# Kernel tuning notes

Measured on AMD Instinct MI355X. Metric: run time of the kernel, lower is better.

The kernel has to match this reference:

```python
import jax, jax.numpy as jnp
import numpy as np

FP8_MAX = 448.0


def _quantize_fp8(x):
    """Per-tensor symmetric quantization matching the Triton kernel's decode.

    Encode: u = round(clip(x*scale, -448, 448) / 448 * 127)  (stored as u+128 in uint8)
    Decode: x_hat = u / 127 * 448 / scale,  with scale = 448 / amax(|x|).
    We keep u as a float array of integers in [-127, 127] (the +128 uint8 bias
    cancels in the kernel's `u - 128`).
    """
    amax = jnp.max(jnp.abs(x))
    scale = FP8_MAX / jnp.maximum(amax, jnp.asarray(1e-12, x.dtype))
    q = jnp.clip(x * scale, -FP8_MAX, FP8_MAX)
    u = jnp.round(q / FP8_MAX * 127.0)
    return u, scale


def reference(x, weight):
    orig_shape = x.shape
    K = weight.shape[1]
    x2d = x.reshape(-1, K)                      # [M, K]

    ua, a_scale = _quantize_fp8(x2d)            # codes + per-tensor scale
    uw, w_scale = _quantize_fp8(weight)         # weight: [N, K]

    # Kernel dequant: val = u / 127 * FP8_MAX; acc in fp32; rescale by 1/(a_scale*b_scale)
    a_f = ua * (FP8_MAX / 127.0)
    b_f = (uw * (FP8_MAX / 127.0)).T            # [K, N] (weight_fp8.t())
    acc = a_f @ b_f                              # fp32 accumulate, [M, N]
    out = acc * (1.0 / (a_scale * w_scale))
    out = out.astype(x.dtype)
    return out.reshape(*orig_shape[:-1], weight.shape[0])


def setup_inputs() -> dict:
    key = jax.random.key(0)
    k1, k2 = jax.random.split(key)
    x = jax.random.normal(k1, (4, 2048, 4096), dtype=jnp.float32)
    weight = jax.random.normal(k2, (8192, 4096), dtype=jnp.float32) * 0.02
    return {"x": x, "weight": weight}
```

## Files before the change

kernel.cpp:

```cpp
#include <hip/hip_runtime.h>

#define FP8_MAX_F 448.0f

static constexpr int M = 8192;
static constexpr int N = 8192;
static constexpr int K = 4096;

typedef __attribute__((ext_vector_type(4))) int i32x4;

#define AS1 __attribute__((address_space(1)))
#define AS3 __attribute__((address_space(3)))
#define BARRIER() asm volatile("s_barrier" ::: "memory")
#define VMCNT(n)  asm volatile("s_waitcnt vmcnt(" #n ")" ::: "memory")

__global__ void amax_kernel(const float* __restrict__ x, const float* __restrict__ w,
                            unsigned* __restrict__ out) {
    const long n4x = (long)M * K / 4;
    const long n4t = n4x + (long)N * K / 4;
    unsigned lx = 0u, lw = 0u;
    const long stride = (long)gridDim.x * blockDim.x;
    for (long i = (long)blockIdx.x * blockDim.x + threadIdx.x; i < n4t; i += stride) {
        if (i < n4x) {
            float4 v = ((const float4*)x)[i];
            unsigned a0 = __float_as_uint(v.x) & 0x7fffffffu;
            unsigned a1 = __float_as_uint(v.y) & 0x7fffffffu;
            unsigned a2 = __float_as_uint(v.z) & 0x7fffffffu;
            unsigned a3 = __float_as_uint(v.w) & 0x7fffffffu;
            lx = max(lx, max(max(a0, a1), max(a2, a3)));
        } else {
            float4 v = ((const float4*)w)[i - n4x];
            unsigned a0 = __float_as_uint(v.x) & 0x7fffffffu;
            unsigned a1 = __float_as_uint(v.y) & 0x7fffffffu;
            unsigned a2 = __float_as_uint(v.z) & 0x7fffffffu;
            unsigned a3 = __float_as_uint(v.w) & 0x7fffffffu;
            lw = max(lw, max(max(a0, a1), max(a2, a3)));
        }
    }
    #pragma unroll
    for (int off = 32; off > 0; off >>= 1) {
        lx = max(lx, (unsigned)__shfl_down((int)lx, off, 64));
        lw = max(lw, (unsigned)__shfl_down((int)lw, off, 64));
    }
    __shared__ unsigned smx[4], smw[4];
    if ((threadIdx.x & 63) == 0) { smx[threadIdx.x >> 6] = lx; smw[threadIdx.x >> 6] = lw; }
    __syncthreads();
    if (threadIdx.x == 0) {
        atomicMax(&out[0], max(max(smx[0], smx[1]), max(smx[2], smx[3])));
        atomicMax(&out[1], max(max(smw[0], smw[1]), max(smw[2], smw[3])));
    }
}

__device__ __forceinline__ signed char quant1(float v, float s) {
    float f = fminf(fmaxf(v * s, -FP8_MAX_F), FP8_MAX_F);
    return (signed char)(int)rintf(f / FP8_MAX_F * 127.0f);
}

__global__ void quant_kernel(const float* __restrict__ x, const float* __restrict__ w,
                             signed char* __restrict__ qx, signed char* __restrict__ qw,
                             const unsigned* __restrict__ amax_bits) {
    const float ax = fmaxf(__uint_as_float(amax_bits[0]), 1e-12f);
    const float aw = fmaxf(__uint_as_float(amax_bits[1]), 1e-12f);
    const float sxv = FP8_MAX_F / ax;
    const float swv = FP8_MAX_F / aw;
    const long cx = (long)M * K / 16;
    const long ct = cx + (long)N * K / 16;
    const long stride = (long)gridDim.x * blockDim.x;
    for (long ci = (long)blockIdx.x * blockDim.x + threadIdx.x; ci < ct; ci += stride) {
        const float* src; signed char* dst; float s; long c;
        if (ci < cx) { src = x; dst = qx; s = sxv; c = ci; }
        else         { src = w; dst = qw; s = swv; c = ci - cx; }
        const long r = c >> 8;
        const int  cr = (int)(c & 255);
        const float4* in = (const float4*)(src + r * K + cr * 16);
        signed char ob[16];
        #pragma unroll
        for (int j = 0; j < 4; ++j) {
            float4 v = in[j];
            ob[j * 4 + 0] = quant1(v.x, s);
            ob[j * 4 + 1] = quant1(v.y, s);
            ob[j * 4 + 2] = quant1(v.z, s);
            ob[j * 4 + 3] = quant1(v.w, s);
        }
        const int osub = (cr & 3) ^ ((int)(r >> 1) & 3);
        *(int4*)(dst + r * K + ((long)((cr & ~3) + osub)) * 16) = *(const int4*)ob;
    }
}

__global__ __launch_bounds__(512, 2) void gemm_i8_kernel(
    const signed char* __restrict__ Aq, const signed char* __restrict__ Bq,
    float* __restrict__ C, const unsigned* __restrict__ amax_bits)
{
    __shared__ signed char lds[4][2][256 * 64];

    const int tid  = threadIdx.x;
    const int wid  = tid >> 6;
    const int lane = tid & 63;
    const int wm = wid >> 2;
    const int wn = wid & 3;
    const int fr = lane & 15;
    const int fq = lane >> 4;

    const long row0 = (long)blockIdx.x * 256;
    const long col0 = (long)blockIdx.y * 256;

    const signed char* Ablk = Aq + row0 * K;
    const signed char* Bblk = Bq + col0 * K;

    const long stag_off = (long)(tid >> 2) * K + (long)(tid & 3) * 16;

    const int arow = wm * 128 + fr;
    const int aoff = arow * 64 + ((fq ^ ((arow >> 1) & 3)) * 16);
    const int brow = wn * 64 + fr;
    const int boff = brow * 64 + ((fq ^ ((brow >> 1) & 3)) * 16);

    i32x4 acc[8][4] = {};

#define STAGE(gbase, lbase) do { \
        __builtin_amdgcn_global_load_lds((const AS1 void*)((gbase) + stag_off), \
            (AS3 void*)((lbase) + wid * 1024), 16, 0, 0); \
        __builtin_amdgcn_global_load_lds((const AS1 void*)((gbase) + stag_off + 128L * K), \
            (AS3 void*)((lbase) + 8192 + wid * 1024), 16, 0, 0); \
    } while (0)

#define MFMA8(nb, bA, bB) do { \
        _Pragma("unroll") \
        for (int mi = 0; mi < 8; ++mi) { \
            acc[mi][nb]     = __builtin_amdgcn_mfma_i32_16x16x64_i8(af[mi], bA, acc[mi][nb], 0, 0, 0); \
            acc[mi][nb + 1] = __builtin_amdgcn_mfma_i32_16x16x64_i8(af[mi], bB, acc[mi][nb + 1], 0, 0, 0); \
        } \
    } while (0)

#define TILE(bufi, STAGE_A_STMT, STAGE_B_STMT, VM_B_STMT) do { \
        const signed char* la = &lds[bufi][0][0]; \
        const signed char* lb = &lds[bufi][1][0]; \
        i32x4 af[8], b0, b1, b2, b3; \
        STAGE_A_STMT; \
        _Pragma("unroll") \
        for (int mi = 0; mi < 8; ++mi) \
            af[mi] = *(const i32x4*)(la + aoff + mi * 1024); \
        b0 = *(const i32x4*)(lb + boff + 0 * 1024); \
        b1 = *(const i32x4*)(lb + boff + 1 * 1024); \
        BARRIER(); \
        __builtin_amdgcn_s_setprio(1); \
        MFMA8(0, b0, b1); \
        __builtin_amdgcn_s_setprio(0); \
        BARRIER(); \
        STAGE_B_STMT; \
        b2 = *(const i32x4*)(lb + boff + 2 * 1024); \
        b3 = *(const i32x4*)(lb + boff + 3 * 1024); \
        VM_B_STMT; \
        BARRIER(); \
        __builtin_amdgcn_s_setprio(1); \
        MFMA8(2, b2, b3); \
        __builtin_amdgcn_s_setprio(0); \
        BARRIER(); \
    } while (0)

    STAGE(Ablk + 0 * 64, &lds[0][0][0]);
    STAGE(Bblk + 0 * 64, &lds[0][1][0]);
    STAGE(Ablk + 1 * 64, &lds[1][0][0]);
    STAGE(Bblk + 1 * 64, &lds[1][1][0]);
    VMCNT(4);
    BARRIER();

    #pragma unroll 1
    for (int t = 0; t <= 60; t += 2) {
        TILE(t & 3,
             STAGE(Ablk + (t + 2) * 64, &lds[(t + 2) & 3][0][0]),
             STAGE(Bblk + (t + 2) * 64, &lds[(t + 2) & 3][1][0]),
             VMCNT(4));
        TILE((t + 1) & 3,
             STAGE(Ablk + (t + 3) * 64, &lds[(t + 3) & 3][0][0]),
             STAGE(Bblk + (t + 3) * 64, &lds[(t + 3) & 3][1][0]),
             VMCNT(4));
    }
    TILE(2, (void)0, (void)0, VMCNT(0));
    TILE(3, (void)0, (void)0, (void)0);

#undef TILE
#undef MFMA8
#undef STAGE

    const float ax = fmaxf(__uint_as_float(amax_bits[0]), 1e-12f);
    const float aw = fmaxf(__uint_as_float(amax_bits[1]), 1e-12f);
    const float factor = ax * aw * (1.0f / (127.0f * 127.0f));

    #pragma unroll
    for (int mi = 0; mi < 8; ++mi) {
        #pragma unroll
        for (int ni = 0; ni < 4; ++ni) {
            const long col = col0 + wn * 64 + ni * 16 + fr;
            #pragma unroll
            for (int j = 0; j < 4; ++j) {
                const long row = row0 + wm * 128 + mi * 16 + fq * 4 + j;
                C[row * N + col] = (float)acc[mi][ni][j] * factor;
            }
        }
    }
}

extern "C" void kernel_launch(void* const* d_in, const int* in_sizes, int n_in,
                              void* d_out, int out_size, void* d_ws, size_t ws_size,
                              hipStream_t stream) {
    const float* x = (const float*)d_in[0];
    const float* w = (const float*)d_in[1];
    float* out = (float*)d_out;

    unsigned char* ws = (unsigned char*)d_ws;
    unsigned* amax = (unsigned*)ws;
    signed char* aq = (signed char*)(ws + 256);
    signed char* wq = aq + (long)M * K;

    hipMemsetAsync(amax, 0, 2 * sizeof(unsigned), stream);
    amax_kernel<<<2048, 256, 0, stream>>>(x, w, amax);
    quant_kernel<<<4096, 256, 0, stream>>>(x, w, aq, wq, amax);

    dim3 grid(M / 256, N / 256);
    gemm_i8_kernel<<<grid, 512, 0, stream>>>(aq, wq, out, amax);
}
```

Baseline: 419.1 us.

## Double-buffer LDS fragments in registers and deepen the global prefetch pipeline

The GEMM main loop now keeps two register sets of A/B fragments, loading the next k-tile's fragments from LDS while the MFMAs consume the current set, and prefetches three k-tiles ahead into the 4-slot LDS ring instead of two. This is meant to hide LDS read latency behind the MFMAs and give the global-to-LDS loads more slack. In exchange it roughly doubles fragment register usage, which risks spills under launch_bounds(512,2). The tail now issues redundant wrapped loads (indices masked with &63) instead of separate epilogue tiles, and the waitcnt depth may not match the deeper prefetch.

After: 419.4 us. About the same (+0.1%).

```diff
diff --git a/kernel.cpp b/kernel.cpp
--- a/kernel.cpp
+++ b/kernel.cpp
@@ -102,7 +102,6 @@
 
     const long row0 = (long)blockIdx.x * 256;
     const long col0 = (long)blockIdx.y * 256;
-
     const signed char* Ablk = Aq + row0 * K;
     const signed char* Bblk = Bq + col0 * K;
 
@@ -114,72 +113,78 @@
     const int boff = brow * 64 + ((fq ^ ((brow >> 1) & 3)) * 16);
 
     i32x4 acc[8][4] = {};
-
-#define STAGE(gbase, lbase) do { \
-        __builtin_amdgcn_global_load_lds((const AS1 void*)((gbase) + stag_off), \
-            (AS3 void*)((lbase) + wid * 1024), 16, 0, 0); \
-        __builtin_amdgcn_global_load_lds((const AS1 void*)((gbase) + stag_off + 128L * K), \
-            (AS3 void*)((lbase) + 8192 + wid * 1024), 16, 0, 0); \
+    i32x4 afR[2][8];
+    i32x4 bR[2][4];
+
+#define STAGE_A(st, bi) do { \
+        const signed char* g = Ablk + (long)(st) * 64 + stag_off; \
+        __builtin_amdgcn_global_load_lds((const AS1 void*)g, \
+            (AS3 void*)(&lds[bi][0][0] + wid * 1024), 16, 0, 0); \
+        __builtin_amdgcn_global_load_lds((const AS1 void*)(g + 128L * K), \
+            (AS3 void*)(&lds[bi][0][0] + 8192 + wid * 1024), 16, 0, 0); \
     } while (0)
 
-#define MFMA8(nb, bA, bB) do { \
-        _Pragma("unroll") \
-        for (int mi = 0; mi < 8; ++mi) { \
-            acc[mi][nb]     = __builtin_amdgcn_mfma_i32_16x16x64_i8(af[mi], bA, acc[mi][nb], 0, 0, 0); \
-            acc[mi][nb + 1] = __builtin_amdgcn_mfma_i32_16x16x64_i8(af[mi], bB, acc[mi][nb + 1], 0, 0, 0); \
-        } \
+#define STAGE_B(st, bi) do { \
+        const signed char* g = Bblk + (long)(st) * 64 + stag_off; \
+        __builtin_amdgcn_global_load_lds((const AS1 void*)g, \
+            (AS3 void*)(&lds[bi][1][0] + wid * 1024), 16, 0, 0); \
+        __builtin_amdgcn_global_load_lds((const AS1 void*)(g + 128L * K), \
+            (AS3 void*)(&lds[bi][1][0] + 8192 + wid * 1024), 16, 0, 0); \
     } while (0)
 
-#define TILE(bufi, STAGE_A_STMT, STAGE_B_STMT, VM_B_STMT) do { \
-        const signed char* la = &lds[bufi][0][0]; \
-        const signed char* lb = &lds[bufi][1][0]; \
-        i32x4 af[8], b0, b1, b2, b3; \
-        STAGE_A_STMT; \
-        _Pragma("unroll") \
-        for (int mi = 0; mi < 8; ++mi) \
-            af[mi] = *(const i32x4*)(la + aoff + mi * 1024); \
-        b0 = *(const i32x4*)(lb + boff + 0 * 1024); \
-        b1 = *(const i32x4*)(lb + boff + 1 * 1024); \
-        BARRIER(); \
-        __builtin_amdgcn_s_setprio(1); \
-        MFMA8(0, b0, b1); \
-        __builtin_amdgcn_s_setprio(0); \
-        BARRIER(); \
-        STAGE_B_STMT; \
-        b2 = *(const i32x4*)(lb + boff + 2 * 1024); \
-        b3 = *(const i32x4*)(lb + boff + 3 * 1024); \
-        VM_B_STMT; \
-        BARRIER(); \
-        __builtin_amdgcn_s_setprio(1); \
-        MFMA8(2, b2, b3); \
-        __builtin_amdgcn_s_setprio(0); \
-        BARRIER(); \
-    } while (0)
-
-    STAGE(Ablk + 0 * 64, &lds[0][0][0]);
-    STAGE(Bblk + 0 * 64, &lds[0][1][0]);
-    STAGE(Ablk + 1 * 64, &lds[1][0][0]);
-    STAGE(Bblk + 1 * 64, &lds[1][1][0]);
+    STAGE_A(0, 0); STAGE_B(0, 0);
+    STAGE_A(1, 1); STAGE_B(1, 1);
+    STAGE_A(2, 2); STAGE_B(2, 2);
     VMCNT(4);
     BARRIER();
+    #pragma unroll
+    for (int mi = 0; mi < 8; ++mi)
+        afR[0][mi] = *(const i32x4*)(&lds[0][0][0] + aoff + mi * 1024);
+    #pragma unroll
+    for (int ni = 0; ni < 4; ++ni)
+        bR[0][ni] = *(const i32x4*)(&lds[0][1][0] + boff + ni * 1024);
+
+#define TILE_BODY(t, CUR, NXT) do { \
+        const signed char* la = &lds[((t) + 1) & 3][0][0]; \
+        const signed char* lb = &lds[((t) + 1) & 3][1][0]; \
+        _Pragma("unroll") \
+        for (int mi = 0; mi < 8; ++mi) \
+            afR[NXT][mi] = *(const i32x4*)(la + aoff + mi * 1024); \
+        STAGE_A(((t) + 3) & 63, ((t) + 3) & 3); \
+        BARRIER(); \
+        __builtin_amdgcn_s_setprio(1); \
+        _Pragma("unroll") \
+        for (int mi = 0; mi < 8; ++mi) { \
+            acc[mi][0] = __builtin_amdgcn_mfma_i32_16x16x64_i8(afR[CUR][mi], bR[CUR][0], acc[mi][0], 0, 0, 0); \
+            acc[mi][1] = __builtin_amdgcn_mfma_i32_16x16x64_i8(afR[CUR][mi], bR[CUR][1], acc[mi][1], 0, 0, 0); \
+        } \
+        __builtin_amdgcn_s_setprio(0); \
+        BARRIER(); \
+        _Pragma("unroll") \
+        for (int ni = 0; ni < 4; ++ni) \
+            bR[NXT][ni] = *(const i32x4*)(lb + boff + ni * 1024); \
+        STAGE_B(((t) + 3) & 63, ((t) + 3) & 3); \
+        VMCNT(4); \
+        BARRIER(); \
+        __builtin_amdgcn_s_setprio(1); \
+        _Pragma("unroll") \
+        for (int mi = 0; mi < 8; ++mi) { \
+            acc[mi][2] = __builtin_amdgcn_mfma_i32_16x16x64_i8(afR[CUR][mi], bR[CUR][2], acc[mi][2], 0, 0, 0); \
+            acc[mi][3] = __builtin_amdgcn_mfma_i32_16x16x64_i8(afR[CUR][mi], bR[CUR][3], acc[mi][3], 0, 0, 0); \
+        } \
+        __builtin_amdgcn_s_setprio(0); \
+        BARRIER(); \
+    } while (0)
 
     #pragma unroll 1
-    for (int t = 0; t <= 60; t += 2) {
-        TILE(t & 3,
-             STAGE(Ablk + (t + 2) * 64, &lds[(t + 2) & 3][0][0]),
-             STAGE(Bblk + (t + 2) * 64, &lds[(t + 2) & 3][1][0]),
-             VMCNT(4));
-        TILE((t + 1) & 3,
-             STAGE(Ablk + (t + 3) * 64, &lds[(t + 3) & 3][0][0]),
-             STAGE(Bblk + (t + 3) * 64, &lds[(t + 3) & 3][1][0]),
-             VMCNT(4));
-    }
-    TILE(2, (void)0, (void)0, VMCNT(0));
-    TILE(3, (void)0, (void)0, (void)0);
-
-#undef TILE
-#undef MFMA8
-#undef STAGE
+    for (int t = 0; t < 64; t += 2) {
+        TILE_BODY(t, 0, 1);
+        TILE_BODY(t + 1, 1, 0);
+    }
+
+#undef TILE_BODY
+#undef STAGE_B
+#undef STAGE_A
 
     const float ax = fmaxf(__uint_as_float(amax_bits[0]), 1e-12f);
     const float aw = fmaxf(__uint_as_float(amax_bits[1]), 1e-12f);
```
